# Optimization experiments

Hardware: AMD Instinct MI355X
Metric: run time of the kernel (lower is better)

The kernel has to match this reference:

```python
import jax, jax.numpy as jnp
import numpy as np

T = 8192          # sequence length
D = 1024          # input_size
H = 16            # n_heads
HEAD = 64         # head_size = hidden_size // n_heads


def setup_inputs() -> dict:
    key = jax.random.key(0)
    ks = jax.random.split(key, 8)
    lim = (1.0 / HEAD) ** 0.5
    u = lambda k, shape: jax.random.uniform(k, shape, minval=-lim, maxval=lim, dtype=jnp.float32)
    return {
        "xs": jax.random.normal(ks[0], (T, D), dtype=jnp.float32),
        "if_weights": u(ks[1], (H, 2, D)),
        "o_weights": u(ks[2], (H, HEAD, D)),
        "kq_weights": u(ks[3], (H, 2 * HEAD, D)),
        "v_weights": u(ks[4], (H, HEAD, D)),
        "if_bias": u(ks[5], (H, 2)),
        "o_bias": u(ks[6], (H, HEAD)),
        "kvq_bias": u(ks[7], (H, 3, HEAD)),
    }


def reference(xs, if_weights, o_weights, kq_weights, v_weights, if_bias, o_bias, kvq_bias):
    inv_sqrt_head = 1.0 / jnp.sqrt(jnp.asarray(HEAD, jnp.float32))

    def step(state, x):
        h_prev, c_prev, m_prev, n_prev = state
        # gates
        i_f = jnp.einsum('htd,d->ht', if_weights, x) + if_bias          # (H, 2)
        o = jax.nn.sigmoid(jnp.einsum('hkd,d->hk', o_weights, x) + o_bias)  # (H, HEAD)
        i, f = i_f[:, 0], i_f[:, 1]
        # log-space stabilizer
        m = jnp.maximum(f + m_prev, i)
        i = jnp.exp(i - m)
        f = jnp.exp(f + m_prev - m)
        # key/query/value projections
        kq = jnp.einsum('hkd,d->hk', kq_weights, x)                      # (H, 2*HEAD)
        k, q = kq[:, :HEAD], kq[:, HEAD:]
        v = jnp.einsum('hkd,d->hk', v_weights, x)
        k = k * inv_sqrt_head + kvq_bias[:, 0]
        v = v + kvq_bias[:, 1]
        q = q + kvq_bias[:, 2]
        # state updates
        n = f[:, None] * n_prev + i[:, None] * k                          # (H, HEAD)
        c = f[:, None, None] * c_prev + i[:, None, None] * (v[:, :, None] * k[:, None, :])  # (H, HEAD, HEAD)
        # readout
        h = jnp.einsum('hij,hj->hi', c, q)                                # (H, HEAD)
        denom = jnp.maximum(jnp.abs(jnp.einsum('hj,hj->h', n, q)), 1.0)  # (H,)
        h = o * (h / denom[:, None])
        return (h, c, m, n), h.reshape(H * HEAD)

    init = (
        jnp.zeros((H, HEAD), jnp.float32),
        jnp.zeros((H, HEAD, HEAD), jnp.float32),
        jnp.zeros((H,), jnp.float32),
        jnp.zeros((H, HEAD), jnp.float32),
    )
    _, hs = jax.lax.scan(step, init, xs)
    return hs  # (T, hidden_size)
```

## Files before the change

kernel.cpp:

```cpp
#include <hip/hip_runtime.h>
#include <math.h>

#define T_LEN 8192
#define D_IN  1024
#define NH    16
#define NPAD  4224
#define NCH   128
#define NGRP  8
#define GSZ   16
#define NPACK 16896
#define NCONV 4096

typedef __attribute__((ext_vector_type(8))) _Float16 f16x8;
typedef __attribute__((ext_vector_type(4))) _Float16 f16x4;
typedef __attribute__((ext_vector_type(4))) float f32x4;

static const size_t OFF_WP   = 0;
static const size_t OFF_BG   = 2300000;
static const size_t OFF_BIAS = OFF_WP + (size_t)NPAD * D_IN;
static const size_t OFF_P    = OFF_BIAS + NPAD;
static const size_t OFF_M    = OFF_P + (size_t)T_LEN * NPAD;
static const size_t OFF_DC   = OFF_M + (size_t)T_LEN * NH;
static const size_t OFF_DN   = OFF_DC + (size_t)NCH * NH * 64 * 64;
static const size_t OFF_DL   = OFF_DN + (size_t)NCH * NH * 64;
static const size_t OFF_IF   = OFF_DL + (size_t)NCH * NH;

__device__ __forceinline__ void glds16(const void* g, void* l) {
  __builtin_amdgcn_global_load_lds(
      (const __attribute__((address_space(1))) void*)g,
      (__attribute__((address_space(3))) void*)l, 16, 0, 0);
}

__global__ __launch_bounds__(256) void pack_conv(
    const float* __restrict__ ifw, const float* __restrict__ ow,
    const float* __restrict__ kqw, const float* __restrict__ vw,
    const float* __restrict__ ifb, const float* __restrict__ ob,
    const float* __restrict__ kvqb, _Float16* __restrict__ Wph,
    float* __restrict__ bias,
    const float* __restrict__ X, _Float16* __restrict__ Xh) {
  int b = blockIdx.x;
  if (b < NPACK) {
    int idx = b * 256 + threadIdx.x;
    int n = idx >> 10, d = idx & 1023;
    float w = 0.f, bb = 0.f;
    if (n < 32) {
      int h = n >> 1, t = n & 1;
      w = ifw[(h * 2 + t) * D_IN + d];
      bb = ifb[h * 2 + t];
    } else if (n < 4128) {
      int r = n - 32;
      int h = r >> 8, j = r & 255;
      if (j < 64)       { w = kqw[(h * 128 + j) * D_IN + d] * 0.125f; bb = kvqb[(h * 3 + 0) * 64 + j]; }
      else if (j < 128) { w = kqw[(h * 128 + j) * D_IN + d];          bb = kvqb[(h * 3 + 2) * 64 + (j - 64)]; }
      else if (j < 192) { w = vw[(h * 64 + (j - 128)) * D_IN + d];    bb = kvqb[(h * 3 + 1) * 64 + (j - 128)]; }
      else              { w = ow[(h * 64 + (j - 192)) * D_IN + d];    bb = ob[h * 64 + (j - 192)]; }
    }
    Wph[(size_t)n * D_IN + d] = (_Float16)w;
    if (d == 0) bias[n] = bb;
  } else {
    int i = ((b - NPACK) * 256 + threadIdx.x) << 3;
    float4 v0 = *(const float4*)(X + i);
    float4 v1 = *(const float4*)(X + i + 4);
    f16x8 r;
    r[0] = (_Float16)v0.x; r[1] = (_Float16)v0.y; r[2] = (_Float16)v0.z; r[3] = (_Float16)v0.w;
    r[4] = (_Float16)v1.x; r[5] = (_Float16)v1.y; r[6] = (_Float16)v1.z; r[7] = (_Float16)v1.w;
    *(f16x8*)(Xh + i) = r;
  }
}

__global__ __launch_bounds__(256) void gemm_f16(
    const _Float16* __restrict__ Xh, const _Float16* __restrict__ Wph,
    const float* __restrict__ bias, _Float16* __restrict__ Ph) {
  __shared__ _Float16 As[2][128 * 32];
  __shared__ _Float16 Bs[2][128 * 32];
  int tid = threadIdx.x;
  int wave = tid >> 6, lane = tid & 63;
  int wgid = blockIdx.x;
  int virt = (wgid & 7) * 264 + (wgid >> 3);
  int mt = virt / 33, nt = virt % 33;
  int m0 = mt << 7, n0 = nt << 7;
  int wr = wave >> 1, wc = wave & 1;

  f32x4 acc[4][4];
  f32x4 zero = {0.f, 0.f, 0.f, 0.f};
#pragma unroll
  for (int i = 0; i < 4; ++i)
#pragma unroll
    for (int j = 0; j < 4; ++j) acc[i][j] = zero;

  int srow = lane >> 2;
  int scol = (lane & 3) << 3;
  const _Float16* ga = Xh + (size_t)(m0 + wave * 32 + srow) * D_IN + scol;
  const _Float16* gb = Wph + (size_t)(n0 + wave * 32 + srow) * D_IN + scol;
  int lds0 = (wave * 32) * 32;
  int lds1 = (wave * 32 + 16) * 32;

  int fr = lane & 15;
  int fk = (lane >> 4) << 3;

  glds16(ga, &As[0][lds0]);
  glds16(ga + 16 * D_IN, &As[0][lds1]);
  glds16(gb, &Bs[0][lds0]);
  glds16(gb + 16 * D_IN, &Bs[0][lds1]);
  __syncthreads();

  int cur = 0;
  for (int k0 = 0; k0 < D_IN; k0 += 32) {
    if (k0 + 32 < D_IN) {
      int kn = k0 + 32;
      glds16(ga + kn, &As[cur ^ 1][lds0]);
      glds16(ga + 16 * D_IN + kn, &As[cur ^ 1][lds1]);
      glds16(gb + kn, &Bs[cur ^ 1][lds0]);
      glds16(gb + 16 * D_IN + kn, &Bs[cur ^ 1][lds1]);
    }
    f16x8 a[4], b[4];
#pragma unroll
    for (int mi = 0; mi < 4; ++mi)
      a[mi] = *(const f16x8*)&As[cur][(wr * 64 + mi * 16 + fr) * 32 + fk];
#pragma unroll
    for (int ni = 0; ni < 4; ++ni)
      b[ni] = *(const f16x8*)&Bs[cur][(wc * 64 + ni * 16 + fr) * 32 + fk];
#pragma unroll
    for (int mi = 0; mi < 4; ++mi)
#pragma unroll
      for (int ni = 0; ni < 4; ++ni)
        acc[mi][ni] = __builtin_amdgcn_mfma_f32_16x16x32_f16(a[mi], b[ni], acc[mi][ni], 0, 0, 0);
    __syncthreads();
    cur ^= 1;
  }

  int cr = (lane >> 4) << 2;
  int cc = lane & 15;
#pragma unroll
  for (int mi = 0; mi < 4; ++mi) {
#pragma unroll
    for (int ni = 0; ni < 4; ++ni) {
      int col = n0 + wc * 64 + ni * 16 + cc;
      float bb = bias[col];
      size_t base = (size_t)(m0 + wr * 64 + mi * 16 + cr) * NPAD + col;
#pragma unroll
      for (int r = 0; r < 4; ++r)
        Ph[base + (size_t)r * NPAD] = (_Float16)(acc[mi][ni][r] + bb);
    }
  }
}

__global__ __launch_bounds__(256) void gemm_if(
    const float* __restrict__ X, const float* __restrict__ ifw,
    const float* __restrict__ ifb, float* __restrict__ IFc) {
  __shared__ float Xs[64 * 72];
  __shared__ float Ws[32 * 68];
  int tid = threadIdx.x;
  int r0 = blockIdx.x << 6;
  int nc = tid & 15;
  int rg = tid >> 4;
  int n0 = nc << 1;
  int sw = ((n0 >> 3) & 3) << 2;
  int sx = (rg & 3) << 2;

  float acc[4][2];
#pragma unroll
  for (int j = 0; j < 4; ++j) { acc[j][0] = 0.f; acc[j][1] = 0.f; }

  for (int k0 = 0; k0 < D_IN; k0 += 64) {
    __syncthreads();
#pragma unroll
    for (int i = 0; i < 4; ++i) {
      int fi = (i << 8) + tid;
      int row = fi >> 4, kk = (fi & 15) << 2;
      float4 v = *(const float4*)(X + (size_t)(r0 + row) * D_IN + k0 + kk);
      *(float4*)&Xs[row * 72 + (kk ^ (((row >> 2) & 3) << 2))] = v;
    }
#pragma unroll
    for (int i = 0; i < 2; ++i) {
      int fi = (i << 8) + tid;
      int row = fi >> 4, kk = (fi & 15) << 2;
      float4 v = *(const float4*)(ifw + (size_t)row * D_IN + k0 + kk);
      *(float4*)&Ws[row * 68 + (kk ^ (((row >> 3) & 3) << 2))] = v;
    }
    __syncthreads();
#pragma unroll
    for (int k4 = 0; k4 < 64; k4 += 4) {
      float4 w0 = *(const float4*)&Ws[n0 * 68 + (k4 ^ sw)];
      float4 w1 = *(const float4*)&Ws[(n0 + 1) * 68 + (k4 ^ sw)];
#pragma unroll
      for (int j = 0; j < 4; ++j) {
        float4 xv = *(const float4*)&Xs[((rg << 2) + j) * 72 + (k4 ^ sx)];
        acc[j][0] = fmaf(xv.x, w0.x, acc[j][0]);
        acc[j][0] = fmaf(xv.y, w0.y, acc[j][0]);
        acc[j][0] = fmaf(xv.z, w0.z, acc[j][0]);
        acc[j][0] = fmaf(xv.w, w0.w, acc[j][0]);
        acc[j][1] = fmaf(xv.x, w1.x, acc[j][1]);
        acc[j][1] = fmaf(xv.y, w1.y, acc[j][1]);
        acc[j][1] = fmaf(xv.z, w1.z, acc[j][1]);
        acc[j][1] = fmaf(xv.w, w1.w, acc[j][1]);
      }
    }
  }
  float b0 = ifb[n0], b1 = ifb[n0 + 1];
#pragma unroll
  for (int j = 0; j < 4; ++j) {
    int row = r0 + (rg << 2) + j;
    float2 st; st.x = acc[j][0] + b0; st.y = acc[j][1] + b1;
    *(float2*)(IFc + ((size_t)row << 5) + n0) = st;
  }
}

__global__ __launch_bounds__(256) void mscan(const float* __restrict__ IFc, float* __restrict__ M) {
  int h = blockIdx.x;
  int tid = threadIdx.x;
  int lane = tid & 63, wv = tid >> 6;
  int t0 = tid << 5;
  float F = 0.f, I = -1e30f;
#pragma unroll 8
  for (int u = 0; u < 32; ++u) {
    float2 v = *(const float2*)(IFc + ((size_t)(t0 + u) << 5) + (h << 1));
    I = fmaxf(I + v.y, v.x);
    F += v.y;
  }
#pragma unroll
  for (int d = 1; d < 64; d <<= 1) {
    float Fo = __shfl_up(F, d, 64);
    float Io = __shfl_up(I, d, 64);
    if (lane >= d) { I = fmaxf(Io + F, I); F = Fo + F; }
  }
  __shared__ float sF[4], sI[4];
  if (lane == 63) { sF[wv] = F; sI[wv] = I; }
  float Fe = __shfl_up(F, 1, 64);
  float Ie = __shfl_up(I, 1, 64);
  if (lane == 0) { Fe = 0.f; Ie = -1e30f; }
  __syncthreads();
  float Fp = 0.f, Ip = -1e30f;
  for (int w = 0; w < wv; ++w) { Ip = fmaxf(Ip + sF[w], sI[w]); Fp += sF[w]; }
  float Ft = Fp + Fe;
  float It = fmaxf(Ip + Fe, Ie);
  float m = fmaxf(Ft, It);
#pragma unroll 8
  for (int u = 0; u < 32; ++u) {
    float2 v = *(const float2*)(IFc + ((size_t)(t0 + u) << 5) + (h << 1));
    m = fmaxf(v.y + m, v.x);
    M[(size_t)(t0 + u) * NH + h] = m;
  }
}

__global__ __launch_bounds__(256) void d1_dc(
    const _Float16* __restrict__ Ph, const float* __restrict__ IFc,
    const float* __restrict__ M,
    _Float16* __restrict__ DCh, float* __restrict__ DN, float* __restrict__ DL) {
  int c = blockIdx.x >> 4, h = blockIdx.x & 15;
  int t0 = c << 6, hb = 32 + (h << 8);
  int tid = threadIdx.x;
  __shared__ float Kl[64][65];
  __shared__ float Vl[64][65];
  __shared__ float gl[64];
#pragma unroll
  for (int i = 0; i < 2; ++i) {
    int fq = (i << 8) + tid;
    int s = fq >> 3, b8 = (fq & 7) << 3;
    const _Float16* row = Ph + (size_t)(t0 + s) * NPAD + hb;
    f16x8 kv = *(const f16x8*)(row + b8);
    f16x8 vv = *(const f16x8*)(row + 128 + b8);
#pragma unroll
    for (int j = 0; j < 8; ++j) {
      Kl[s][b8 + j] = (float)kv[j];
      Vl[s][b8 + j] = (float)vv[j];
    }
  }
  if (tid < 64) {
    float2 iff = *(const float2*)(IFc + ((size_t)(t0 + tid) << 5) + (h << 1));
    float iv = iff.x, fv = iff.y;
    float cs = fv;
#pragma unroll
    for (int dd = 1; dd < 64; dd <<= 1) {
      float o = __shfl_up(cs, dd, 64);
      cs += (tid >= dd) ? o : 0.f;
    }
    float cumL = __shfl(cs, 63, 64);
    float mL = M[(size_t)(t0 + 63) * NH + h];
    gl[tid] = __expf(cumL - cs + iv - mL);
    if (tid == 0) {
      float mstart = (c > 0) ? M[(size_t)(t0 - 1) * NH + h] : 0.f;
      DL[(c << 4) + h] = __expf(mstart + cumL - mL);
    }
  }
  __syncthreads();
  if (tid < 64) {
    float acc = 0.f;
#pragma unroll
    for (int s = 0; s < 64; ++s) acc = fmaf(gl[s], Kl[s][tid], acc);
    DN[((size_t)(c << 4) + h) * 64 + tid] = acc;
  }
  int a = tid & 63, bq = tid >> 6;
  float acc[16];
#pragma unroll
  for (int j = 0; j < 16; ++j) acc[j] = 0.f;
  for (int s = 0; s < 64; ++s) {
    float gv = gl[s] * Vl[s][a];
#pragma unroll
    for (int j = 0; j < 16; ++j) acc[j] = fmaf(gv, Kl[s][(bq << 4) + j], acc[j]);
  }
  size_t base = (((size_t)(c << 4) + h) << 12) + ((size_t)a << 6) + (bq << 4);
  f16x8 s0, s1;
#pragma unroll
  for (int j = 0; j < 8; ++j) { s0[j] = (_Float16)acc[j]; s1[j] = (_Float16)acc[8 + j]; }
  *(f16x8*)(DCh + base) = s0;
  *(f16x8*)(DCh + base + 8) = s1;
}

__global__ __launch_bounds__(256) void d2a(
    const _Float16* __restrict__ DCh, const float* __restrict__ DN,
    const float* __restrict__ DL,
    float* __restrict__ BgDC, float* __restrict__ BgDN, float* __restrict__ Ag) {
  int bid = blockIdx.x, tid = threadIdx.x;
  if (bid < 2048) {
    int linear = (bid << 8) + tid;
    int g = linear >> 16, e = linear & 65535;
    int h = e >> 12;
    float carry = 0.f, a = 1.f;
    size_t idx = (size_t)e + ((size_t)g << 4) * 65536;
    float v = (float)DCh[idx];
    for (int u = 0; u < GSZ; ++u) {
      float dl = DL[(((g << 4) + u) << 4) + h];
      float vn = (u < GSZ - 1) ? (float)DCh[idx + 65536] : 0.f;
      carry = fmaf(dl, carry, v);
      a *= dl;
      v = vn;
      idx += 65536;
    }
    BgDC[((size_t)g << 16) + e] = carry;
    if ((e & 4095) == 0) Ag[(g << 4) + h] = a;
  } else {
    int linear = ((bid - 2048) << 8) + tid;
    int g = linear >> 10, e = linear & 1023;
    int h = e >> 6;
    float carry = 0.f;
    size_t idx = (size_t)e + ((size_t)g << 4) * 1024;
    float v = DN[idx];
    for (int u = 0; u < GSZ; ++u) {
      float dl = DL[(((g << 4) + u) << 4) + h];
      float vn = (u < GSZ - 1) ? DN[idx + 1024] : 0.f;
      carry = fmaf(dl, carry, v);
      v = vn;
      idx += 1024;
    }
    BgDN[(g << 10) + e] = carry;
  }
}

__global__ __launch_bounds__(256) void d2c(
    _Float16* __restrict__ DCh, float* __restrict__ DN,
    const float* __restrict__ DL,
    const float* __restrict__ BgDC, const float* __restrict__ BgDN,
    const float* __restrict__ Ag) {
  int bid = blockIdx.x, tid = threadIdx.x;
  if (bid < 2048) {
    int linear = (bid << 8) + tid;
    int g = linear >> 16, e = linear & 65535;
    int h = e >> 12;
    float P = 0.f;
    for (int gp = 0; gp < g; ++gp)
      P = fmaf(Ag[(gp << 4) + h], P, BgDC[((size_t)gp << 16) + e]);
    float carry = P;
    size_t idx = (size_t)e + ((size_t)g << 4) * 65536;
    float v = (float)DCh[idx];
    for (int u = 0; u < GSZ; ++u) {
      float dl = DL[(((g << 4) + u) << 4) + h];
      float vn = (u < GSZ - 1) ? (float)DCh[idx + 65536] : 0.f;
      DCh[idx] = (_Float16)carry;
      carry = fmaf(dl, carry, v);
      v = vn;
      idx += 65536;
    }
  } else {
    int linear = ((bid - 2048) << 8) + tid;
    int g = linear >> 10, e = linear & 1023;
    int h = e >> 6;
    float P = 0.f;
    for (int gp = 0; gp < g; ++gp)
      P = fmaf(Ag[(gp << 4) + h], P, BgDN[(gp << 10) + e]);
    float carry = P;
    size_t idx = (size_t)e + ((size_t)g << 4) * 1024;
    float v = DN[idx];
    for (int u = 0; u < GSZ; ++u) {
      float dl = DL[(((g << 4) + u) << 4) + h];
      float vn = (u < GSZ - 1) ? DN[idx + 1024] : 0.f;
      DN[idx] = carry;
      carry = fmaf(dl, carry, v);
      v = vn;
      idx += 1024;
    }
  }
}

__global__ __launch_bounds__(256) void d3_out(
    const _Float16* __restrict__ Ph, const float* __restrict__ IFc,
    const float* __restrict__ M,
    const _Float16* __restrict__ CS, const float* __restrict__ NS,
    float* __restrict__ out) {
  int c = blockIdx.x >> 4, h = blockIdx.x & 15;
  int t0 = c << 6, hb = 32 + (h << 8);
  int tid = threadIdx.x;
  int lane = tid & 63, wave = tid >> 6;
  __shared__ _Float16 Kh[64 * 72];
  __shared__ _Float16 Qh[64 * 72];
  __shared__ _Float16 Vt[64 * 72];
  __shared__ _Float16 Ch[64 * 72];
  __shared__ _Float16 Oh[64 * 72];
  __shared__ _Float16 Pl[64 * 72];
  __shared__ float cf[64], il[64], ml[64], dl[64], nq[64], nsl[64];

#pragma unroll
  for (int i = 0; i < 2; ++i) {
    int fq = (i << 8) + tid;
    int s = fq >> 3, b8 = (fq & 7) << 3;
    const _Float16* row = Ph + (size_t)(t0 + s) * NPAD + hb;
    f16x8 kv = *(const f16x8*)(row + b8);
    f16x8 qv = *(const f16x8*)(row + 64 + b8);
    f16x8 vv = *(const f16x8*)(row + 128 + b8);
    f16x8 ov = *(const f16x8*)(row + 192 + b8);
    f16x8 cv = *(const f16x8*)(CS + ((((size_t)(c << 4)) + h) << 12) + ((size_t)s << 6) + b8);
    *(f16x8*)&Kh[s * 72 + b8] = kv;
    *(f16x8*)&Qh[s * 72 + b8] = qv;
    *(f16x8*)&Oh[s * 72 + b8] = ov;
    *(f16x8*)&Ch[s * 72 + b8] = cv;
#pragma unroll
    for (int j = 0; j < 8; ++j) Vt[(b8 + j) * 72 + s] = vv[j];
  }
  __syncthreads();

  float iv = 0.f, mt = 0.f, cs = 0.f;
  if (tid < 64) {
    float2 iff = *(const float2*)(IFc + ((size_t)(t0 + tid) << 5) + (h << 1));
    iv = iff.x;
    float fv = iff.y;
    mt = M[(size_t)(t0 + tid) * NH + h];
    nsl[tid] = NS[((size_t)(c << 4) + h) * 64 + tid];
    cs = fv;
#pragma unroll
    for (int dd = 1; dd < 64; dd <<= 1) {
      float o = __shfl_up(cs, dd, 64);
      cs += (tid >= dd) ? o : 0.f;
    }
  }
  __syncthreads();
  if (tid < 64) {
    cf[tid] = cs; il[tid] = iv; ml[tid] = mt;
    float mstart = (c > 0) ? M[(size_t)(t0 - 1) * NH + h] : 0.f;
    dl[tid] = __expf(mstart + cs - mt);
    float acc = 0.f;
#pragma unroll
    for (int b = 0; b < 64; ++b) acc = fmaf(nsl[b], (float)Qh[tid * 72 + b], acc);
    nq[tid] = acc;
  }
  __syncthreads();

  int band = wave << 4;
  int arow = lane & 15;
  int kq = (lane >> 4) << 3;
  int crow = (lane >> 4) << 2;

  f16x8 aq0 = *(const f16x8*)&Qh[(band + arow) * 72 + kq];
  f16x8 aq1 = *(const f16x8*)&Qh[(band + arow) * 72 + 32 + kq];

  f32x4 S[4];
  f32x4 zero = {0.f, 0.f, 0.f, 0.f};
#pragma unroll
  for (int n = 0; n < 4; ++n) S[n] = zero;
#pragma unroll
  for (int n = 0; n < 4; ++n) {
    f16x8 b0 = *(const f16x8*)&Kh[((n << 4) + arow) * 72 + kq];
    f16x8 b1 = *(const f16x8*)&Kh[((n << 4) + arow) * 72 + 32 + kq];
    S[n] = __builtin_amdgcn_mfma_f32_16x16x32_f16(aq0, b0, S[n], 0, 0, 0);
    S[n] = __builtin_amdgcn_mfma_f32_16x16x32_f16(aq1, b1, S[n], 0, 0, 0);
  }

  float cft[4], mlt[4];
#pragma unroll
  for (int r = 0; r < 4; ++r) {
    int t = band + crow + r;
    cft[r] = cf[t]; mlt[r] = ml[t];
  }
  float rsum[4] = {0.f, 0.f, 0.f, 0.f};
#pragma unroll
  for (int n = 0; n < 4; ++n) {
    int s = (n << 4) + arow;
    float cfs = cf[s], ils = il[s];
#pragma unroll
    for (int r = 0; r < 4; ++r) {
      int t = band + crow + r;
      float w = (s <= t) ? __expf(cft[r] - cfs + ils - mlt[r]) : 0.f;
      float p = S[n][r] * w;
      rsum[r] += p;
      Pl[t * 72 + s] = (_Float16)p;
    }
  }
#pragma unroll
  for (int r = 0; r < 4; ++r) {
    float p = rsum[r];
    p += __shfl_xor(p, 1);
    p += __shfl_xor(p, 2);
    p += __shfl_xor(p, 4);
    p += __shfl_xor(p, 8);
    rsum[r] = p;
  }
  __syncthreads();

  f16x8 ap0 = *(const f16x8*)&Pl[(band + arow) * 72 + kq];
  f16x8 ap1 = *(const f16x8*)&Pl[(band + arow) * 72 + 32 + kq];
  f32x4 H[4], I[4];
#pragma unroll
  for (int n = 0; n < 4; ++n) { H[n] = zero; I[n] = zero; }
#pragma unroll
  for (int n = 0; n < 4; ++n) {
    f16x8 bv0 = *(const f16x8*)&Vt[((n << 4) + arow) * 72 + kq];
    f16x8 bv1 = *(const f16x8*)&Vt[((n << 4) + arow) * 72 + 32 + kq];
    H[n] = __builtin_amdgcn_mfma_f32_16x16x32_f16(ap0, bv0, H[n], 0, 0, 0);
    H[n] = __builtin_amdgcn_mfma_f32_16x16x32_f16(ap1, bv1, H[n], 0, 0, 0);
    f16x8 bc0 = *(const f16x8*)&Ch[((n << 4) + arow) * 72 + kq];
    f16x8 bc1 = *(const f16x8*)&Ch[((n << 4) + arow) * 72 + 32 + kq];
    I[n] = __builtin_amdgcn_mfma_f32_16x16x32_f16(aq0, bc0, I[n], 0, 0, 0);
    I[n] = __builtin_amdgcn_mfma_f32_16x16x32_f16(aq1, bc1, I[n], 0, 0, 0);
  }

#pragma unroll
  for (int r = 0; r < 4; ++r) {
    int t = band + crow + r;
    float dt = dl[t];
    float dn = fmaf(dt, nq[t], rsum[r]);
    float rinv = 1.f / fmaxf(fabsf(dn), 1.f);
    float* orow = out + (size_t)(t0 + t) * 1024 + (h << 6);
#pragma unroll
    for (int n = 0; n < 4; ++n) {
      int a = (n << 4) + arow;
      float o = 1.f / (1.f + __expf(-(float)Oh[t * 72 + a]));
      orow[a] = o * (fmaf(dt, I[n][r], H[n][r]) * rinv);
    }
  }
}

extern "C" void kernel_launch(void* const* d_in, const int* in_sizes, int n_in,
                              void* d_out, int out_size, void* d_ws, size_t ws_size,
                              hipStream_t stream) {
  const float* xs   = (const float*)d_in[0];
  const float* ifw  = (const float*)d_in[1];
  const float* ow   = (const float*)d_in[2];
  const float* kqw  = (const float*)d_in[3];
  const float* vw   = (const float*)d_in[4];
  const float* ifb  = (const float*)d_in[5];
  const float* ob   = (const float*)d_in[6];
  const float* kvqb = (const float*)d_in[7];
  float* ws   = (float*)d_ws;
  _Float16* Wph = (_Float16*)(ws + OFF_WP);
  float* BgDC = ws + OFF_BG;
  float* BgDN = BgDC + (size_t)NGRP * 65536;
  float* Ag   = BgDN + (size_t)NGRP * 1024;
  float* bias = ws + OFF_BIAS;
  _Float16* Phm = (_Float16*)(ws + OFF_P);
  float* Mm   = ws + OFF_M;
  _Float16* DCh = (_Float16*)(ws + OFF_DC);
  _Float16* Xh  = (_Float16*)(ws + OFF_DC);
  float* DN   = ws + OFF_DN;
  float* DL   = ws + OFF_DL;
  float* IFc  = ws + OFF_IF;
  float* outp = (float*)d_out;

  hipLaunchKernelGGL(pack_conv, dim3(NPACK + NCONV), dim3(256), 0, stream,
                     ifw, ow, kqw, vw, ifb, ob, kvqb, Wph, bias, xs, Xh);
  hipLaunchKernelGGL(gemm_f16, dim3(33 * 64), dim3(256), 0, stream,
                     Xh, Wph, bias, Phm);
  hipLaunchKernelGGL(gemm_if, dim3(T_LEN / 64), dim3(256), 0, stream, xs, ifw, ifb, IFc);
  hipLaunchKernelGGL(mscan, dim3(NH), dim3(256), 0, stream, IFc, Mm);
  hipLaunchKernelGGL(d1_dc, dim3(NCH * NH), dim3(256), 0, stream, Phm, IFc, Mm, DCh, DN, DL);
  hipLaunchKernelGGL(d2a, dim3(2080), dim3(256), 0, stream, DCh, DN, DL, BgDC, BgDN, Ag);
  hipLaunchKernelGGL(d2c, dim3(2080), dim3(256), 0, stream, DCh, DN, DL, BgDC, BgDN, Ag);
  hipLaunchKernelGGL(d3_out, dim3(NCH * NH), dim3(256), 0, stream, Phm, IFc, Mm, DCh, DN, outp);
}
```

Measured before the change: 244.7 us.

## Rework f16 projection GEMM with 128x256 tiles, swizzled LDS and deeper pipelining

Replaces the 128x128, 256-thread projection GEMM with a 512-thread 128x256 tile. It splits K into half-stages across a two-slot LDS ring with XOR-swizzled columns to avoid bank conflicts. Loads are issued ahead with explicit vmcnt waits, raw barriers, sched_barrier and setprio around the MFMA bursts to overlap global-to-LDS traffic with compute. The weight matrix is padded to 4352 rows so the wider N tiles divide evenly, at the cost of some wasted MFMA work on padding columns and dummy loads at the tail to keep the wait counts uniform.

```diff
diff --git a/kernel.cpp b/kernel.cpp
--- a/kernel.cpp
+++ b/kernel.cpp
@@ -5,10 +5,11 @@
 #define D_IN  1024
 #define NH    16
 #define NPAD  4224
+#define NWROW 4352
 #define NCH   128
 #define NGRP  8
 #define GSZ   16
-#define NPACK 16896
+#define NPACK 17408
 #define NCONV 4096
 
 typedef __attribute__((ext_vector_type(8))) _Float16 f16x8;
@@ -17,7 +18,7 @@
 
 static const size_t OFF_WP   = 0;
 static const size_t OFF_BG   = 2300000;
-static const size_t OFF_BIAS = OFF_WP + (size_t)NPAD * D_IN;
+static const size_t OFF_BIAS = (size_t)NPAD * D_IN;
 static const size_t OFF_P    = OFF_BIAS + NPAD;
 static const size_t OFF_M    = OFF_P + (size_t)T_LEN * NPAD;
 static const size_t OFF_DC   = OFF_M + (size_t)T_LEN * NH;
@@ -56,7 +57,7 @@
       else              { w = ow[(h * 64 + (j - 192)) * D_IN + d];    bb = ob[h * 64 + (j - 192)]; }
     }
     Wph[(size_t)n * D_IN + d] = (_Float16)w;
-    if (d == 0) bias[n] = bb;
+    if (d == 0 && n < NPAD) bias[n] = bb;
   } else {
     int i = ((b - NPACK) * 256 + threadIdx.x) << 3;
     float4 v0 = *(const float4*)(X + i);
@@ -68,18 +69,27 @@
   }
 }
 
-__global__ __launch_bounds__(256) void gemm_f16(
+__global__ __launch_bounds__(512, 2) void gemm_f16(
     const _Float16* __restrict__ Xh, const _Float16* __restrict__ Wph,
     const float* __restrict__ bias, _Float16* __restrict__ Ph) {
-  __shared__ _Float16 As[2][128 * 32];
-  __shared__ _Float16 Bs[2][128 * 32];
+  __shared__ _Float16 As[2][2][128 * 32];
+  __shared__ _Float16 Bs[2][2][256 * 32];
+  __shared__ _Float16 Dm[8192];
   int tid = threadIdx.x;
   int wave = tid >> 6, lane = tid & 63;
-  int wgid = blockIdx.x;
-  int virt = (wgid & 7) * 264 + (wgid >> 3);
-  int mt = virt / 33, nt = virt % 33;
-  int m0 = mt << 7, n0 = nt << 7;
-  int wr = wave >> 1, wc = wave & 1;
+  int wr = wave >> 2, wc = wave & 3;
+
+  int virt = (blockIdx.x & 7) * 136 + (blockIdx.x >> 3);
+  int bm0 = (virt & 63) << 7;
+  int bn0 = (virt >> 6) << 8;
+
+  int sRow = wave * 16 + (lane >> 2);
+  int scol = (((lane & 3) ^ ((lane >> 3) & 3)) << 3);
+  const _Float16* gA = Xh + (size_t)(bm0 + sRow) * D_IN + scol;
+  const _Float16* gB = Wph + (size_t)(bn0 + sRow) * D_IN + scol;
+
+  int fr = lane & 15;
+  int fko = (((lane >> 4) ^ ((fr >> 1) & 3)) << 3);
 
   f32x4 acc[4][4];
   f32x4 zero = {0.f, 0.f, 0.f, 0.f};
@@ -88,46 +98,56 @@
 #pragma unroll
     for (int j = 0; j < 4; ++j) acc[i][j] = zero;
 
-  int srow = lane >> 2;
-  int scol = (lane & 3) << 3;
-  const _Float16* ga = Xh + (size_t)(m0 + wave * 32 + srow) * D_IN + scol;
-  const _Float16* gb = Wph + (size_t)(n0 + wave * 32 + srow) * D_IN + scol;
-  int lds0 = (wave * 32) * 32;
-  int lds1 = (wave * 32 + 16) * 32;
-
-  int fr = lane & 15;
-  int fk = (lane >> 4) << 3;
-
-  glds16(ga, &As[0][lds0]);
-  glds16(ga + 16 * D_IN, &As[0][lds1]);
-  glds16(gb, &Bs[0][lds0]);
-  glds16(gb + 16 * D_IN, &Bs[0][lds1]);
-  __syncthreads();
-
-  int cur = 0;
-  for (int k0 = 0; k0 < D_IN; k0 += 32) {
-    if (k0 + 32 < D_IN) {
-      int kn = k0 + 32;
-      glds16(ga + kn, &As[cur ^ 1][lds0]);
-      glds16(ga + 16 * D_IN + kn, &As[cur ^ 1][lds1]);
-      glds16(gb + kn, &Bs[cur ^ 1][lds0]);
-      glds16(gb + 16 * D_IN + kn, &Bs[cur ^ 1][lds1]);
-    }
-    f16x8 a[4], b[4];
-#pragma unroll
-    for (int mi = 0; mi < 4; ++mi)
-      a[mi] = *(const f16x8*)&As[cur][(wr * 64 + mi * 16 + fr) * 32 + fk];
-#pragma unroll
-    for (int ni = 0; ni < 4; ++ni)
-      b[ni] = *(const f16x8*)&Bs[cur][(wc * 64 + ni * 16 + fr) * 32 + fk];
-#pragma unroll
-    for (int mi = 0; mi < 4; ++mi)
-#pragma unroll
-      for (int ni = 0; ni < 4; ++ni)
-        acc[mi][ni] = __builtin_amdgcn_mfma_f32_16x16x32_f16(a[mi], b[ni], acc[mi][ni], 0, 0, 0);
-    __syncthreads();
-    cur ^= 1;
-  }
+#define STAGE(TT, KH) do {                                                   \
+    int tt_ = (TT), kh_ = (KH);                                              \
+    if (tt_ < 16) {                                                          \
+      int sl_ = tt_ & 1;                                                     \
+      int ko_ = tt_ * 64 + kh_ * 32;                                         \
+      glds16(gA + ko_, &As[sl_][kh_][wave * 512]);                           \
+      glds16(gB + ko_, &Bs[sl_][kh_][wave * 512]);                           \
+      glds16(gB + (size_t)128 * D_IN + ko_, &Bs[sl_][kh_][4096 + wave * 512]);\
+    } else {                                                                 \
+      glds16(gA, &Dm[wave * 512]);                                           \
+      glds16(gA, &Dm[4096 + wave * 512]);                                    \
+      glds16(gA, &Dm[wave * 512]);                                           \
+    }                                                                        \
+  } while (0)
+
+#define COMPUTE(SL, KH) do {                                                 \
+    f16x8 av[4], bv[4];                                                      \
+    _Pragma("unroll")                                                        \
+    for (int mi = 0; mi < 4; ++mi)                                           \
+      av[mi] = *(const f16x8*)&As[SL][KH][(wr * 64 + mi * 16 + fr) * 32 + fko];\
+    _Pragma("unroll")                                                        \
+    for (int ni = 0; ni < 4; ++ni)                                           \
+      bv[ni] = *(const f16x8*)&Bs[SL][KH][(wc * 64 + ni * 16 + fr) * 32 + fko];\
+    asm volatile("s_waitcnt vmcnt(6)" ::: "memory");                         \
+    __builtin_amdgcn_s_barrier();                                            \
+    __builtin_amdgcn_sched_barrier(0);                                       \
+    __builtin_amdgcn_s_setprio(1);                                           \
+    _Pragma("unroll")                                                        \
+    for (int mi = 0; mi < 4; ++mi)                                           \
+      _Pragma("unroll")                                                      \
+      for (int ni = 0; ni < 4; ++ni)                                         \
+        acc[mi][ni] = __builtin_amdgcn_mfma_f32_16x16x32_f16(av[mi], bv[ni], acc[mi][ni], 0, 0, 0);\
+    __builtin_amdgcn_s_setprio(0);                                           \
+    __builtin_amdgcn_sched_barrier(0);                                       \
+  } while (0)
+
+  STAGE(0, 0); STAGE(0, 1); STAGE(1, 0);
+  asm volatile("s_waitcnt vmcnt(6)" ::: "memory");
+  __builtin_amdgcn_s_barrier();
+  __builtin_amdgcn_sched_barrier(0);
+
+  for (int i = 0; i < 8; ++i) {
+    int t0 = i << 1;
+    STAGE(t0 + 1, 1); COMPUTE(0, 0);
+    STAGE(t0 + 2, 0); COMPUTE(0, 1);
+    STAGE(t0 + 2, 1); COMPUTE(1, 0);
+    STAGE(t0 + 3, 0); COMPUTE(1, 1);
+  }
+#undef STAGE
+#undef COMPUTE
 
   int cr = (lane >> 4) << 2;
   int cc = lane & 15;
@@ -135,12 +155,14 @@
   for (int mi = 0; mi < 4; ++mi) {
 #pragma unroll
     for (int ni = 0; ni < 4; ++ni) {
-      int col = n0 + wc * 64 + ni * 16 + cc;
-      float bb = bias[col];
-      size_t base = (size_t)(m0 + wr * 64 + mi * 16 + cr) * NPAD + col;
-#pragma unroll
-      for (int r = 0; r < 4; ++r)
-        Ph[base + (size_t)r * NPAD] = (_Float16)(acc[mi][ni][r] + bb);
+      int col = bn0 + wc * 64 + ni * 16 + cc;
+      if (col < NPAD) {
+        float bb = bias[col];
+        size_t base = (size_t)(bm0 + wr * 64 + mi * 16 + cr) * NPAD + col;
+#pragma unroll
+        for (int r = 0; r < 4; ++r)
+          Ph[base + (size_t)r * NPAD] = (_Float16)(acc[mi][ni][r] + bb);
+      }
     }
   }
 }
@@ -566,7 +588,7 @@
 
   hipLaunchKernelGGL(pack_conv, dim3(NPACK + NCONV), dim3(256), 0, stream,
                      ifw, ow, kqw, vw, ifb, ob, kvqb, Wph, bias, xs, Xh);
-  hipLaunchKernelGGL(gemm_f16, dim3(33 * 64), dim3(256), 0, stream,
+  hipLaunchKernelGGL(gemm_f16, dim3(64 * 17), dim3(512), 0, stream,
                      Xh, Wph, bias, Phm);
   hipLaunchKernelGGL(gemm_if, dim3(T_LEN / 64), dim3(256), 0, stream, xs, ifw, ifb, IFc);
   hipLaunchKernelGGL(mscan, dim3(NH), dim3(256), 0, stream, IFc, Mm);
```

Measured after the change: 280.7 us. +14.7%, slower.
